# Kernel tuning notes

Hardware: AMD Instinct MI355X
Metric: run time of the kernel (lower is better)

Reference implementation:

```python
import jax, jax.numpy as jnp
import numpy as np

DIM = 4096
NUM_HEAD = 32
NUM_KV_HEAD = 8
ROPE_THETA = 10000.0
B, T = 2, 2048


def apply_rope(x, start_pos=0, theta=ROPE_THETA):
    # x: [B, T, H, d_head]; rotate half-split pairs by position-dependent angles
    d = x.shape[-1]
    half = d // 2
    inv_freq = 1.0 / (theta ** (jnp.arange(0, half, dtype=jnp.float32) / half))
    pos = jnp.arange(x.shape[1], dtype=jnp.float32) + start_pos  # [T]
    ang = pos[:, None] * inv_freq[None, :]                       # [T, half]
    cos = jnp.cos(ang)[None, :, None, :]
    sin = jnp.sin(ang)[None, :, None, :]
    x1, x2 = x[..., :half], x[..., half:]
    return jnp.concatenate([x1 * cos - x2 * sin, x1 * sin + x2 * cos], axis=-1)


def setup_inputs() -> dict:
    key = jax.random.key(0)
    ks = jax.random.split(key, 5)
    scale = 0.02
    X = jax.random.normal(ks[0], (B, T, DIM), dtype=jnp.float32)
    Wq = jax.random.normal(ks[1], (DIM, DIM), dtype=jnp.float32) * scale
    Wk = jax.random.normal(ks[2], (DIM, DIM // NUM_HEAD * NUM_KV_HEAD), dtype=jnp.float32) * scale
    Wv = jax.random.normal(ks[3], (DIM, DIM // NUM_HEAD * NUM_KV_HEAD), dtype=jnp.float32) * scale
    Wo = jax.random.normal(ks[4], (DIM, DIM), dtype=jnp.float32) * scale
    return {"X": X, "Wq": Wq, "Wk": Wk, "Wv": Wv, "Wo": Wo}


def reference(X, Wq, Wk, Wv, Wo):
    Bs, Ts, C = X.shape
    H, Hkv = NUM_HEAD, NUM_KV_HEAD
    dh = C // H
    G = H // Hkv  # GQA group size

    Q = apply_rope((X @ Wq).reshape(Bs, Ts, H, dh))      # [B,T,H,dh]
    K = apply_rope((X @ Wk).reshape(Bs, Ts, Hkv, dh))    # [B,T,Hkv,dh]
    V = (X @ Wv).reshape(Bs, Ts, Hkv, dh)                # [B,T,Hkv,dh]

    # [B,Hkv,G,T,dh]: grouped layout equivalent to repeat_interleave on head dim
    Qh = Q.transpose(0, 2, 1, 3).reshape(Bs, Hkv, G, Ts, dh)
    Kh = K.transpose(0, 2, 1, 3)  # [B,Hkv,T,dh]
    Vh = V.transpose(0, 2, 1, 3)

    scores = jnp.einsum('bkgtd,bksd->bkgts', Qh, Kh) / jnp.sqrt(jnp.float32(dh))
    causal = jnp.tril(jnp.ones((Ts, Ts), dtype=bool))
    scores = jnp.where(causal[None, None, None], scores, -jnp.inf)
    attn = jax.nn.softmax(scores, axis=-1)
    out = jnp.einsum('bkgts,bksd->bkgtd', attn, Vh)       # [B,Hkv,G,T,dh]
    out = out.reshape(Bs, H, Ts, dh).transpose(0, 2, 1, 3).reshape(Bs, Ts, C)
    return out @ Wo
```

## Files before the change

kernel.cpp:

```cpp
#include <hip/hip_runtime.h>
#include <hip/hip_bf16.h>
#include <cstdint>
#include <cstddef>

#define B_   2
#define T_   2048
#define DIM_ 4096
#define H_   32
#define HKV_ 8
#define DH_  128
#define MROWS (B_*T_)

typedef __bf16 bf16_t;
typedef bf16_t bf16x8 __attribute__((ext_vector_type(8)));
typedef bf16_t bf16x4 __attribute__((ext_vector_type(4)));
typedef float  f32x4  __attribute__((ext_vector_type(4)));

typedef __attribute__((address_space(1))) void gvoid_t;
typedef __attribute__((address_space(3))) void lvoid_t;

__device__ __forceinline__ void gld_lds16(const void* g, void* l) {
  __builtin_amdgcn_global_load_lds((gvoid_t*)g, (lvoid_t*)l, 16, 0, 0);
}

__device__ __forceinline__ f32x4 mfma16(bf16x8 a, bf16x8 b, f32x4 c) {
  return __builtin_amdgcn_mfma_f32_16x16x32_bf16(a, b, c, 0, 0, 0);
}

__global__ void cast_f32_bf16(const float* __restrict__ in,
                              bf16_t* __restrict__ out, int n4) {
  int i = blockIdx.x * blockDim.x + threadIdx.x;
  if (i < n4) {
    float4 v = ((const float4*)in)[i];
    bf16x4 o;
    o[0] = (bf16_t)v.x; o[1] = (bf16_t)v.y; o[2] = (bf16_t)v.z; o[3] = (bf16_t)v.w;
    ((bf16x4*)out)[i] = o;
  }
}

__global__ void transpose_cast(const float* __restrict__ in,
                               bf16_t* __restrict__ out, int K, int N) {
  __shared__ float tile[32][33];
  int n0 = blockIdx.x * 32, k0 = blockIdx.y * 32;
  int tx = threadIdx.x, ty = threadIdx.y;
#pragma unroll
  for (int j = 0; j < 4; ++j)
    tile[ty + j*8][tx] = in[(size_t)(k0 + ty + j*8) * N + n0 + tx];
  __syncthreads();
#pragma unroll
  for (int j = 0; j < 4; ++j)
    out[(size_t)(n0 + ty + j*8) * K + k0 + tx] = (bf16_t)tile[tx][ty + j*8];
}

template <int OUT_F32>
__global__ __launch_bounds__(256, 2)
void gemm_bt(const bf16_t* __restrict__ A, const bf16_t* __restrict__ BT,
             void* __restrict__ C, int M, int N, int K) {
  __shared__ __align__(16) bf16_t Als[128 * 32];
  __shared__ __align__(16) bf16_t Bls[128 * 32];
  const int tid  = threadIdx.x;
  const int wave = tid >> 6, lane = tid & 63;
  const int quad = lane >> 4, l16 = lane & 15;
  const int wm = wave >> 1, wn = wave & 1;
  const int m0 = blockIdx.y * 128, n0 = blockIdx.x * 128;

  f32x4 acc[4][4] = {};

  const int srow = lane >> 2;
  const int scol = (lane & 3) * 8;

  for (int k0 = 0; k0 < K; k0 += 32) {
#pragma unroll
    for (int c = 0; c < 2; ++c) {
      int ch = wave * 2 + c;
      gld_lds16(A + (size_t)(m0 + ch*16 + srow) * K + k0 + scol,
                &Als[ch*512 + srow*32 + scol]);
    }
#pragma unroll
    for (int c = 0; c < 2; ++c) {
      int ch = wave * 2 + c;
      gld_lds16(BT + (size_t)(n0 + ch*16 + srow) * K + k0 + scol,
                &Bls[ch*512 + srow*32 + scol]);
    }
    __syncthreads();

    bf16x8 af[4], bfr[4];
#pragma unroll
    for (int mi = 0; mi < 4; ++mi)
      af[mi] = *(const bf16x8*)&Als[(wm*64 + mi*16 + l16)*32 + quad*8];
#pragma unroll
    for (int ni = 0; ni < 4; ++ni)
      bfr[ni] = *(const bf16x8*)&Bls[(wn*64 + ni*16 + l16)*32 + quad*8];
#pragma unroll
    for (int mi = 0; mi < 4; ++mi)
#pragma unroll
      for (int ni = 0; ni < 4; ++ni)
        acc[mi][ni] = mfma16(af[mi], bfr[ni], acc[mi][ni]);
    __syncthreads();
  }

#pragma unroll
  for (int mi = 0; mi < 4; ++mi)
#pragma unroll
    for (int ni = 0; ni < 4; ++ni)
#pragma unroll
      for (int r = 0; r < 4; ++r) {
        int row = m0 + wm*64 + mi*16 + quad*4 + r;
        int col = n0 + wn*64 + ni*16 + l16;
        if (OUT_F32)
          ((float*)C)[(size_t)row * N + col] = acc[mi][ni][r];
        else
          ((bf16_t*)C)[(size_t)row * N + col] = (bf16_t)acc[mi][ni][r];
      }
}

__global__ void rope_kernel(bf16_t* __restrict__ X, int Hn, int total) {
  int i = blockIdx.x * blockDim.x + threadIdx.x;
  if (i >= total) return;
  int d   = i & 63;
  int rem = i >> 6;
  int h   = rem % Hn; rem /= Hn;
  int t   = rem % T_;
  int b   = rem / T_;
  size_t base = ((size_t)(b * T_ + t) * Hn + h) * DH_;
  float x1 = (float)X[base + d];
  float x2 = (float)X[base + 64 + d];
  float inv_freq = expf(-(float)d * 0.14391156758f);
  float ang = (float)t * inv_freq;
  float s, c;
  sincosf(ang, &s, &c);
  X[base + d]      = (bf16_t)(x1 * c - x2 * s);
  X[base + 64 + d] = (bf16_t)(x1 * s + x2 * c);
}

__global__ void v_transpose(const bf16_t* __restrict__ Vb,
                            bf16_t* __restrict__ VT) {
  __shared__ bf16_t tile[32][33];
  int t0 = blockIdx.x * 32;
  int d0 = blockIdx.y * 32;
  int bk = blockIdx.z;
  int b = bk >> 3, kv = bk & 7;
  int tx = threadIdx.x, ty = threadIdx.y;
#pragma unroll
  for (int j = 0; j < 4; ++j)
    tile[ty + j*8][tx] =
        Vb[(size_t)(b * T_ + t0 + ty + j*8) * (HKV_*DH_) + kv*DH_ + d0 + tx];
  __syncthreads();
#pragma unroll
  for (int j = 0; j < 4; ++j)
    VT[((size_t)bk * DH_ + d0 + ty + j*8) * T_ + t0 + tx] = tile[tx][ty + j*8];
}

__global__ __launch_bounds__(256, 2)
void flash_attn(const bf16_t* __restrict__ Qb, const bf16_t* __restrict__ Kb,
                const bf16_t* __restrict__ VT, bf16_t* __restrict__ Ob) {
  __shared__ __align__(16) bf16_t Kls[64 * 128];
  __shared__ __align__(16) bf16_t Vls[128 * 64];
  __shared__ __align__(16) bf16_t Pls[128 * 72];

  const int tid = threadIdx.x, wave = tid >> 6, lane = tid & 63;
  const int quad = lane >> 4, l16 = lane & 15;
  const int qt = blockIdx.x, h = blockIdx.y, b = blockIdx.z;
  const int kv = h >> 2;

  bf16x8 q[2][4];
#pragma unroll
  for (int mi = 0; mi < 2; ++mi) {
    const bf16_t* base =
        Qb + (size_t)(b*T_ + qt*128 + wave*32 + mi*16 + l16) * DIM_ + h*DH_;
#pragma unroll
    for (int kk = 0; kk < 4; ++kk)
      q[mi][kk] = *(const bf16x8*)(base + kk*32 + quad*8);
  }

  float m_st[2][4], l_st[2][4];
  f32x4 o_acc[2][8] = {};
#pragma unroll
  for (int mi = 0; mi < 2; ++mi)
#pragma unroll
    for (int r = 0; r < 4; ++r) { m_st[mi][r] = -3e38f; l_st[mi][r] = 0.f; }

  const int nkv = 2 * (qt + 1);
  for (int kvt = 0; kvt < nkv; ++kvt) {
    __syncthreads();

    {
      int r_in = lane >> 4, cphys = lane & 15;
#pragma unroll
      for (int c = 0; c < 4; ++c) {
        int ch = wave * 4 + c;
        int krow = ch * 4 + r_in;
        int clog = cphys ^ (krow & 7);
        gld_lds16(Kb + (size_t)(b*T_ + kvt*64 + krow) * (HKV_*DH_) + kv*DH_ + clog*8,
                  &Kls[ch*512 + lane*8]);
      }
      int r8 = lane >> 3, c8 = lane & 7;
#pragma unroll
      for (int c = 0; c < 4; ++c) {
        int ch = wave * 4 + c;
        int drow = ch * 8 + r8;
        int clog = c8 ^ (drow & 7);
        gld_lds16(VT + ((size_t)(b*HKV_ + kv) * DH_ + drow) * T_ + kvt*64 + clog*8,
                  &Vls[ch*512 + lane*8]);
      }
    }
    __syncthreads();

    f32x4 s[2][4] = {};
#pragma unroll
    for (int kk = 0; kk < 4; ++kk) {
      bf16x8 kf[4];
#pragma unroll
      for (int ni = 0; ni < 4; ++ni) {
        int krow = ni*16 + l16;
        int cphys = (kk*4 + quad) ^ (krow & 7);
        kf[ni] = *(const bf16x8*)&Kls[krow*128 + cphys*8];
      }
#pragma unroll
      for (int mi = 0; mi < 2; ++mi)
#pragma unroll
        for (int ni = 0; ni < 4; ++ni)
          s[mi][ni] = mfma16(q[mi][kk], kf[ni], s[mi][ni]);
    }

    const float sc = 0.08838834764831845f;
    const bool need_mask = (kvt >= 2*qt);
#pragma unroll
    for (int mi = 0; mi < 2; ++mi) {
      float al[4];
#pragma unroll
      for (int r = 0; r < 4; ++r) {
        int rpos = qt*128 + wave*32 + mi*16 + quad*4 + r;
        float mx = -3e38f;
#pragma unroll
        for (int ni = 0; ni < 4; ++ni) {
          float v = s[mi][ni][r] * sc;
          if (need_mask) {
            int cpos = kvt*64 + ni*16 + l16;
            if (cpos > rpos) v = -3e38f;
          }
          s[mi][ni][r] = v;
          mx = fmaxf(mx, v);
        }
#pragma unroll
        for (int off = 1; off < 16; off <<= 1)
          mx = fmaxf(mx, __shfl_xor(mx, off, 64));
        float mnew = fmaxf(m_st[mi][r], mx);
        float alpha = __expf(m_st[mi][r] - mnew);
        m_st[mi][r] = mnew;
        float rs = 0.f;
#pragma unroll
        for (int ni = 0; ni < 4; ++ni) {
          float p = __expf(s[mi][ni][r] - mnew);
          s[mi][ni][r] = p;
          rs += p;
        }
#pragma unroll
        for (int off = 1; off < 16; off <<= 1)
          rs += __shfl_xor(rs, off, 64);
        l_st[mi][r] = l_st[mi][r] * alpha + rs;
        al[r] = alpha;
      }
#pragma unroll
      for (int ni = 0; ni < 8; ++ni)
#pragma unroll
        for (int r = 0; r < 4; ++r) o_acc[mi][ni][r] *= al[r];
#pragma unroll
      for (int ni = 0; ni < 4; ++ni)
#pragma unroll
        for (int r = 0; r < 4; ++r) {
          int prow = wave*32 + mi*16 + quad*4 + r;
          Pls[prow*72 + ni*16 + l16] = (bf16_t)s[mi][ni][r];
        }
    }
    __syncthreads();

#pragma unroll
    for (int kk = 0; kk < 2; ++kk) {
      bf16x8 pf[2], vf[8];
#pragma unroll
      for (int mi = 0; mi < 2; ++mi) {
        int prow = wave*32 + mi*16 + l16;
        pf[mi] = *(const bf16x8*)&Pls[prow*72 + kk*32 + quad*8];
      }
#pragma unroll
      for (int ni = 0; ni < 8; ++ni) {
        int drow = ni*16 + l16;
        int cphys = (kk*4 + quad) ^ (drow & 7);
        vf[ni] = *(const bf16x8*)&Vls[drow*64 + cphys*8];
      }
#pragma unroll
      for (int mi = 0; mi < 2; ++mi)
#pragma unroll
        for (int ni = 0; ni < 8; ++ni)
          o_acc[mi][ni] = mfma16(pf[mi], vf[ni], o_acc[mi][ni]);
    }
  }

#pragma unroll
  for (int mi = 0; mi < 2; ++mi) {
    float inv[4];
#pragma unroll
    for (int r = 0; r < 4; ++r) inv[r] = 1.f / l_st[mi][r];
#pragma unroll
    for (int ni = 0; ni < 8; ++ni)
#pragma unroll
      for (int r = 0; r < 4; ++r) {
        size_t row = (size_t)(b*T_ + qt*128 + wave*32 + mi*16 + quad*4 + r);
        int col = h*DH_ + ni*16 + l16;
        Ob[row * DIM_ + col] = (bf16_t)(o_acc[mi][ni][r] * inv[r]);
      }
  }
}

extern "C" void kernel_launch(void* const* d_in, const int* in_sizes, int n_in,
                              void* d_out, int out_size, void* d_ws, size_t ws_size,
                              hipStream_t stream) {
  const float* X  = (const float*)d_in[0];
  const float* Wq = (const float*)d_in[1];
  const float* Wk = (const float*)d_in[2];
  const float* Wv = (const float*)d_in[3];
  const float* Wo = (const float*)d_in[4];
  float* out = (float*)d_out;

  char* ws = (char*)d_ws;
  const size_t SZ_X  = (size_t)MROWS * DIM_ * 2;
  const size_t SZ_WQ = (size_t)DIM_ * DIM_ * 2;
  const size_t SZ_WK = (size_t)DIM_ * 1024 * 2;
  bf16_t* Xb  = (bf16_t*)(ws);
  bf16_t* WqT = (bf16_t*)(ws + SZ_X);
  bf16_t* WkT = (bf16_t*)(ws + SZ_X + SZ_WQ);
  bf16_t* WvT = (bf16_t*)(ws + SZ_X + SZ_WQ + SZ_WK);
  bf16_t* WoT = (bf16_t*)(ws + SZ_X + SZ_WQ + 2*SZ_WK);
  bf16_t* Qb  = (bf16_t*)(ws + SZ_X + 2*SZ_WQ + 2*SZ_WK);
  bf16_t* Kb  = (bf16_t*)(ws + 2*SZ_X + 2*SZ_WQ + 2*SZ_WK);
  bf16_t* Vb  = (bf16_t*)(ws + 2*SZ_X + 2*SZ_WQ + 3*SZ_WK);
  bf16_t* VT  = (bf16_t*)(ws + 2*SZ_X + 2*SZ_WQ + 4*SZ_WK);
  bf16_t* Ob  = Xb;

  {
    int n4 = MROWS * DIM_ / 4;
    cast_f32_bf16<<<(n4 + 255)/256, 256, 0, stream>>>(X, Xb, n4);
  }
  transpose_cast<<<dim3(DIM_/32, DIM_/32), dim3(32,8), 0, stream>>>(Wq, WqT, DIM_, DIM_);
  transpose_cast<<<dim3(1024/32, DIM_/32), dim3(32,8), 0, stream>>>(Wk, WkT, DIM_, 1024);
  transpose_cast<<<dim3(1024/32, DIM_/32), dim3(32,8), 0, stream>>>(Wv, WvT, DIM_, 1024);
  transpose_cast<<<dim3(DIM_/32, DIM_/32), dim3(32,8), 0, stream>>>(Wo, WoT, DIM_, DIM_);

  gemm_bt<0><<<dim3(DIM_/128, MROWS/128), 256, 0, stream>>>(Xb, WqT, Qb, MROWS, DIM_, DIM_);
  gemm_bt<0><<<dim3(1024/128, MROWS/128), 256, 0, stream>>>(Xb, WkT, Kb, MROWS, 1024, DIM_);
  gemm_bt<0><<<dim3(1024/128, MROWS/128), 256, 0, stream>>>(Xb, WvT, Vb, MROWS, 1024, DIM_);

  {
    int totq = B_ * T_ * H_ * 64;
    rope_kernel<<<(totq + 255)/256, 256, 0, stream>>>(Qb, H_, totq);
    int totk = B_ * T_ * HKV_ * 64;
    rope_kernel<<<(totk + 255)/256, 256, 0, stream>>>(Kb, HKV_, totk);
  }

  v_transpose<<<dim3(T_/32, DH_/32, B_*HKV_), dim3(32,8), 0, stream>>>(Vb, VT);

  flash_attn<<<dim3(T_/128, H_, B_), 256, 0, stream>>>(Qb, Kb, VT, Ob);

  gemm_bt<1><<<dim3(DIM_/128, MROWS/128), 256, 0, stream>>>(Ob, WoT, out, MROWS, DIM_, DIM_);
}
```

Before: 993.7 us.

## Fuse QKV projections into one GEMM and restructure flash attention

```diff
diff --git a/kernel.cpp b/kernel.cpp
--- a/kernel.cpp
+++ b/kernel.cpp
@@ -10,14 +10,24 @@
 #define HKV_ 8
 #define DH_  128
 #define MROWS (B_*T_)
+#define QS_   6144
+#define KOFF_ 4096
+#define VOFF_ 5120
 
 typedef __bf16 bf16_t;
 typedef bf16_t bf16x8 __attribute__((ext_vector_type(8)));
 typedef bf16_t bf16x4 __attribute__((ext_vector_type(4)));
+typedef bf16_t bf16x2 __attribute__((ext_vector_type(2)));
 typedef float  f32x4  __attribute__((ext_vector_type(4)));
 
 typedef __attribute__((address_space(1))) void gvoid_t;
 typedef __attribute__((address_space(3))) void lvoid_t;
+
+#if __has_builtin(__builtin_amdgcn_exp2f)
+#define EXP2F(x) __builtin_amdgcn_exp2f(x)
+#else
+#define EXP2F(x) exp2f(x)
+#endif
 
 __device__ __forceinline__ void gld_lds16(const void* g, void* l) {
   __builtin_amdgcn_global_load_lds((gvoid_t*)g, (lvoid_t*)l, 16, 0, 0);
@@ -65,7 +75,6 @@
   const int m0 = blockIdx.y * 128, n0 = blockIdx.x * 128;
 
   f32x4 acc[4][4] = {};
-
   const int srow = lane >> 2;
   const int scol = (lane & 3) * 8;
 
@@ -114,7 +123,8 @@
       }
 }
 
-__global__ void rope_kernel(bf16_t* __restrict__ X, int Hn, int total) {
+__global__ void rope_kernel(bf16_t* __restrict__ X, int Hn, int rowStr,
+                            int headOff, int total) {
   int i = blockIdx.x * blockDim.x + threadIdx.x;
   if (i >= total) return;
   int d   = i & 63;
@@ -122,7 +132,7 @@
   int h   = rem % Hn; rem /= Hn;
   int t   = rem % T_;
   int b   = rem / T_;
-  size_t base = ((size_t)(b * T_ + t) * Hn + h) * DH_;
+  size_t base = (size_t)(b * T_ + t) * rowStr + headOff + h * DH_;
   float x1 = (float)X[base + d];
   float x2 = (float)X[base + 64 + d];
   float inv_freq = expf(-(float)d * 0.14391156758f);
@@ -133,7 +143,7 @@
   X[base + 64 + d] = (bf16_t)(x1 * s + x2 * c);
 }
 
-__global__ void v_transpose(const bf16_t* __restrict__ Vb,
+__global__ void v_transpose(const bf16_t* __restrict__ Vin,
                             bf16_t* __restrict__ VT) {
   __shared__ bf16_t tile[32][33];
   int t0 = blockIdx.x * 32;
@@ -144,62 +154,57 @@
 #pragma unroll
   for (int j = 0; j < 4; ++j)
     tile[ty + j*8][tx] =
-        Vb[(size_t)(b * T_ + t0 + ty + j*8) * (HKV_*DH_) + kv*DH_ + d0 + tx];
+        Vin[(size_t)(b * T_ + t0 + ty + j*8) * QS_ + kv*DH_ + d0 + tx];
   __syncthreads();
 #pragma unroll
   for (int j = 0; j < 4; ++j)
     VT[((size_t)bk * DH_ + d0 + ty + j*8) * T_ + t0 + tx] = tile[tx][ty + j*8];
 }
 
-__global__ __launch_bounds__(256, 2)
-void flash_attn(const bf16_t* __restrict__ Qb, const bf16_t* __restrict__ Kb,
-                const bf16_t* __restrict__ VT, bf16_t* __restrict__ Ob) {
+__global__ __launch_bounds__(256, 3)
+void flash_attn(const bf16_t* __restrict__ QKV, const bf16_t* __restrict__ VT,
+                bf16_t* __restrict__ Ob) {
   __shared__ __align__(16) bf16_t Kls[64 * 128];
   __shared__ __align__(16) bf16_t Vls[128 * 64];
-  __shared__ __align__(16) bf16_t Pls[128 * 72];
 
   const int tid = threadIdx.x, wave = tid >> 6, lane = tid & 63;
   const int quad = lane >> 4, l16 = lane & 15;
-  const int qt = blockIdx.x, h = blockIdx.y, b = blockIdx.z;
+  const int idx = blockIdx.x;
+  const int qt = 15 - (idx & 15);
+  const int h  = (idx >> 4) & 31;
+  const int b  = idx >> 9;
   const int kv = h >> 2;
 
+  const float CSC = 0.12751744642f;
+
   bf16x8 q[2][4];
 #pragma unroll
-  for (int mi = 0; mi < 2; ++mi) {
+  for (int qb = 0; qb < 2; ++qb) {
     const bf16_t* base =
-        Qb + (size_t)(b*T_ + qt*128 + wave*32 + mi*16 + l16) * DIM_ + h*DH_;
+        QKV + (size_t)(b*T_ + qt*128 + wave*32 + qb*16 + l16) * QS_ + h*DH_;
 #pragma unroll
     for (int kk = 0; kk < 4; ++kk)
-      q[mi][kk] = *(const bf16x8*)(base + kk*32 + quad*8);
-  }
-
-  float m_st[2][4], l_st[2][4];
-  f32x4 o_acc[2][8] = {};
-#pragma unroll
-  for (int mi = 0; mi < 2; ++mi)
-#pragma unroll
-    for (int r = 0; r < 4; ++r) { m_st[mi][r] = -3e38f; l_st[mi][r] = 0.f; }
+      q[qb][kk] = *(const bf16x8*)(base + kk*32 + quad*8);
+  }
+
+  float m_st[2] = {-3e38f, -3e38f}, l_st[2] = {0.f, 0.f};
+  f32x4 o_acc[8][2] = {};
 
   const int nkv = 2 * (qt + 1);
   for (int kvt = 0; kvt < nkv; ++kvt) {
     __syncthreads();
-
     {
-      int r_in = lane >> 4, cphys = lane & 15;
+      int r_in = lane >> 4, cph = lane & 15;
 #pragma unroll
       for (int c = 0; c < 4; ++c) {
-        int ch = wave * 4 + c;
-        int krow = ch * 4 + r_in;
-        int clog = cphys ^ (krow & 7);
-        gld_lds16(Kb + (size_t)(b*T_ + kvt*64 + krow) * (HKV_*DH_) + kv*DH_ + clog*8,
+        int ch = wave*4 + c, krow = ch*4 + r_in, clog = cph ^ (krow & 7);
+        gld_lds16(QKV + (size_t)(b*T_ + kvt*64 + krow) * QS_ + KOFF_ + kv*DH_ + clog*8,
                   &Kls[ch*512 + lane*8]);
       }
       int r8 = lane >> 3, c8 = lane & 7;
 #pragma unroll
       for (int c = 0; c < 4; ++c) {
-        int ch = wave * 4 + c;
-        int drow = ch * 8 + r8;
-        int clog = c8 ^ (drow & 7);
+        int ch = wave*4 + c, drow = ch*8 + r8, clog = c8 ^ (drow & 7);
         gld_lds16(VT + ((size_t)(b*HKV_ + kv) * DH_ + drow) * T_ + kvt*64 + clog*8,
                   &Vls[ch*512 + lane*8]);
       }
@@ -211,104 +216,108 @@
     for (int kk = 0; kk < 4; ++kk) {
       bf16x8 kf[4];
 #pragma unroll
-      for (int ni = 0; ni < 4; ++ni) {
-        int krow = ni*16 + l16;
-        int cphys = (kk*4 + quad) ^ (krow & 7);
-        kf[ni] = *(const bf16x8*)&Kls[krow*128 + cphys*8];
-      }
-#pragma unroll
-      for (int mi = 0; mi < 2; ++mi)
-#pragma unroll
-        for (int ni = 0; ni < 4; ++ni)
-          s[mi][ni] = mfma16(q[mi][kk], kf[ni], s[mi][ni]);
-    }
-
-    const float sc = 0.08838834764831845f;
+      for (int nb = 0; nb < 4; ++nb) {
+        int krow = nb*16 + l16;
+        int pc = (kk*4 + quad) ^ (krow & 7);
+        kf[nb] = *(const bf16x8*)&Kls[krow*128 + pc*8];
+      }
+#pragma unroll
+      for (int qb = 0; qb < 2; ++qb)
+#pragma unroll
+        for (int nb = 0; nb < 4; ++nb)
+          s[qb][nb] = mfma16(kf[nb], q[qb][kk], s[qb][nb]);
+    }
+
     const bool need_mask = (kvt >= 2*qt);
-#pragma unroll
-    for (int mi = 0; mi < 2; ++mi) {
-      float al[4];
-#pragma unroll
-      for (int r = 0; r < 4; ++r) {
-        int rpos = qt*128 + wave*32 + mi*16 + quad*4 + r;
-        float mx = -3e38f;
-#pragma unroll
-        for (int ni = 0; ni < 4; ++ni) {
-          float v = s[mi][ni][r] * sc;
-          if (need_mask) {
-            int cpos = kvt*64 + ni*16 + l16;
-            if (cpos > rpos) v = -3e38f;
-          }
-          s[mi][ni][r] = v;
-          mx = fmaxf(mx, v);
-        }
-#pragma unroll
-        for (int off = 1; off < 16; off <<= 1)
-          mx = fmaxf(mx, __shfl_xor(mx, off, 64));
-        float mnew = fmaxf(m_st[mi][r], mx);
-        float alpha = __expf(m_st[mi][r] - mnew);
-        m_st[mi][r] = mnew;
-        float rs = 0.f;
-#pragma unroll
-        for (int ni = 0; ni < 4; ++ni) {
-          float p = __expf(s[mi][ni][r] - mnew);
-          s[mi][ni][r] = p;
+    union PU { uint32_t u[4]; bf16x8 v; };
+    PU pb[2][2];
+
+#pragma unroll
+    for (int qb = 0; qb < 2; ++qb) {
+      if (need_mask) {
+        int qpos = qt*128 + wave*32 + qb*16 + l16;
+#pragma unroll
+        for (int nb = 0; nb < 4; ++nb)
+#pragma unroll
+          for (int r = 0; r < 4; ++r)
+            if (kvt*64 + nb*16 + quad*4 + r > qpos) s[qb][nb][r] = -3e38f;
+      }
+      float mx = -3e38f;
+#pragma unroll
+      for (int nb = 0; nb < 4; ++nb)
+#pragma unroll
+        for (int r = 0; r < 4; ++r) mx = fmaxf(mx, s[qb][nb][r]);
+      mx = fmaxf(mx, __shfl_xor(mx, 16, 64));
+      mx = fmaxf(mx, __shfl_xor(mx, 32, 64));
+      float mnew = fmaxf(m_st[qb], mx);
+      float alpha = EXP2F((m_st[qb] - mnew) * CSC);
+      m_st[qb] = mnew;
+      float mc = mnew * CSC;
+      float rs = 0.f;
+#pragma unroll
+      for (int nb = 0; nb < 4; ++nb)
+#pragma unroll
+        for (int r = 0; r < 4; ++r) {
+          float p = EXP2F(fmaf(s[qb][nb][r], CSC, -mc));
+          s[qb][nb][r] = p;
           rs += p;
         }
-#pragma unroll
-        for (int off = 1; off < 16; off <<= 1)
-          rs += __shfl_xor(rs, off, 64);
-        l_st[mi][r] = l_st[mi][r] * alpha + rs;
-        al[r] = alpha;
-      }
-#pragma unroll
-      for (int ni = 0; ni < 8; ++ni)
-#pragma unroll
-        for (int r = 0; r < 4; ++r) o_acc[mi][ni][r] *= al[r];
-#pragma unroll
-      for (int ni = 0; ni < 4; ++ni)
-#pragma unroll
-        for (int r = 0; r < 4; ++r) {
-          int prow = wave*32 + mi*16 + quad*4 + r;
-          Pls[prow*72 + ni*16 + l16] = (bf16_t)s[mi][ni][r];
+      rs += __shfl_xor(rs, 16, 64);
+      rs += __shfl_xor(rs, 32, 64);
+      l_st[qb] = l_st[qb] * alpha + rs;
+#pragma unroll
+      for (int dhb = 0; dhb < 8; ++dhb) o_acc[dhb][qb] *= alpha;
+
+      uint32_t pk2[4][2];
+#pragma unroll
+      for (int nb = 0; nb < 4; ++nb)
+#pragma unroll
+        for (int rp = 0; rp < 2; ++rp) {
+          union BU { bf16x2 v; uint32_t u; } bu;
+          bu.v[0] = (bf16_t)s[qb][nb][2*rp];
+          bu.v[1] = (bf16_t)s[qb][nb][2*rp+1];
+          pk2[nb][rp] = bu.u;
         }
-    }
-    __syncthreads();
-
-#pragma unroll
-    for (int kk = 0; kk < 2; ++kk) {
-      bf16x8 pf[2], vf[8];
-#pragma unroll
-      for (int mi = 0; mi < 2; ++mi) {
-        int prow = wave*32 + mi*16 + l16;
-        pf[mi] = *(const bf16x8*)&Pls[prow*72 + kk*32 + quad*8];
-      }
-#pragma unroll
-      for (int ni = 0; ni < 8; ++ni) {
-        int drow = ni*16 + l16;
-        int cphys = (kk*4 + quad) ^ (drow & 7);
-        vf[ni] = *(const bf16x8*)&Vls[drow*64 + cphys*8];
-      }
-#pragma unroll
-      for (int mi = 0; mi < 2; ++mi)
-#pragma unroll
-        for (int ni = 0; ni < 8; ++ni)
-          o_acc[mi][ni] = mfma16(pf[mi], vf[ni], o_acc[mi][ni]);
-    }
-  }
-
-#pragma unroll
-  for (int mi = 0; mi < 2; ++mi) {
-    float inv[4];
-#pragma unroll
-    for (int r = 0; r < 4; ++r) inv[r] = 1.f / l_st[mi][r];
-#pragma unroll
-    for (int ni = 0; ni < 8; ++ni)
-#pragma unroll
-      for (int r = 0; r < 4; ++r) {
-        size_t row = (size_t)(b*T_ + qt*128 + wave*32 + mi*16 + quad*4 + r);
-        int col = h*DH_ + ni*16 + l16;
-        Ob[row * DIM_ + col] = (bf16_t)(o_acc[mi][ni][r] * inv[r]);
+#pragma unroll
+      for (int kb = 0; kb < 2; ++kb)
+#pragma unroll
+        for (int k = 0; k < 4; ++k) {
+          uint32_t x = pk2[2*kb + ((quad & 1) ^ (k >> 1))][k & 1];
+          int src = (2*(quad & 1) + ((k >> 1) ^ (quad >> 1))) * 16 + l16;
+          uint32_t got = (uint32_t)__shfl((int)x, src, 64);
+          pb[qb][kb].u[k ^ ((quad >> 1) << 1)] = got;
+        }
+    }
+
+#pragma unroll
+    for (int dhb = 0; dhb < 8; ++dhb) {
+      bf16x8 vf[2];
+      int drow = dhb*16 + l16;
+#pragma unroll
+      for (int kb = 0; kb < 2; ++kb) {
+        int pc = (kb*4 + quad) ^ (drow & 7);
+        vf[kb] = *(const bf16x8*)&Vls[drow*64 + pc*8];
+      }
+#pragma unroll
+      for (int qb = 0; qb < 2; ++qb)
+#pragma unroll
+        for (int kb = 0; kb < 2; ++kb)
+          o_acc[dhb][qb] = mfma16(vf[kb], pb[qb][kb].v, o_acc[dhb][qb]);
+    }
+  }
+
+#pragma unroll
+  for (int qb = 0; qb < 2; ++qb) {
+    float inv = 1.f / l_st[qb];
+    size_t qrow = (size_t)(b*T_ + qt*128 + wave*32 + qb*16 + l16);
+#pragma unroll
+    for (int dhb = 0; dhb < 8; ++dhb)
+#pragma unroll
+      for (int rp = 0; rp < 2; ++rp) {
+        union BU { bf16x2 v; uint32_t u; } bu;
+        bu.v[0] = (bf16_t)(o_acc[dhb][qb][2*rp]   * inv);
+        bu.v[1] = (bf16_t)(o_acc[dhb][qb][2*rp+1] * inv);
+        *(uint32_t*)(Ob + qrow*DIM_ + h*DH_ + dhb*16 + quad*4 + 2*rp) = bu.u;
       }
   }
 }
@@ -324,43 +333,38 @@
   float* out = (float*)d_out;
 
   char* ws = (char*)d_ws;
-  const size_t SZ_X  = (size_t)MROWS * DIM_ * 2;
-  const size_t SZ_WQ = (size_t)DIM_ * DIM_ * 2;
-  const size_t SZ_WK = (size_t)DIM_ * 1024 * 2;
-  bf16_t* Xb  = (bf16_t*)(ws);
-  bf16_t* WqT = (bf16_t*)(ws + SZ_X);
-  bf16_t* WkT = (bf16_t*)(ws + SZ_X + SZ_WQ);
-  bf16_t* WvT = (bf16_t*)(ws + SZ_X + SZ_WQ + SZ_WK);
-  bf16_t* WoT = (bf16_t*)(ws + SZ_X + SZ_WQ + 2*SZ_WK);
-  bf16_t* Qb  = (bf16_t*)(ws + SZ_X + 2*SZ_WQ + 2*SZ_WK);
-  bf16_t* Kb  = (bf16_t*)(ws + 2*SZ_X + 2*SZ_WQ + 2*SZ_WK);
-  bf16_t* Vb  = (bf16_t*)(ws + 2*SZ_X + 2*SZ_WQ + 3*SZ_WK);
-  bf16_t* VT  = (bf16_t*)(ws + 2*SZ_X + 2*SZ_WQ + 4*SZ_WK);
-  bf16_t* Ob  = Xb;
+  const size_t SZ_X    = (size_t)MROWS * DIM_ * 2;
+  const size_t SZ_WQKV = (size_t)QS_ * DIM_ * 2;
+  const size_t SZ_WO   = (size_t)DIM_ * DIM_ * 2;
+  const size_t SZ_QKV  = (size_t)MROWS * QS_ * 2;
+  bf16_t* Xb    = (bf16_t*)(ws);
+  bf16_t* WT    = (bf16_t*)(ws + SZ_X);
+  bf16_t* WoT   = (bf16_t*)(ws + SZ_X + SZ_WQKV);
+  bf16_t* QKVb  = (bf16_t*)(ws + SZ_X + SZ_WQKV + SZ_WO);
+  bf16_t* VT    = (bf16_t*)(ws + SZ_X + SZ_WQKV + SZ_WO + SZ_QKV);
+  bf16_t* Ob    = Xb;
 
   {
     int n4 = MROWS * DIM_ / 4;
     cast_f32_bf16<<<(n4 + 255)/256, 256, 0, stream>>>(X, Xb, n4);
   }
-  transpose_cast<<<dim3(DIM_/32, DIM_/32), dim3(32,8), 0, stream>>>(Wq, WqT, DIM_, DIM_);
-  transpose_cast<<<dim3(1024/32, DIM_/32), dim3(32,8), 0, stream>>>(Wk, WkT, DIM_, 1024);
-  transpose_cast<<<dim3(1024/32, DIM_/32), dim3(32,8), 0, stream>>>(Wv, WvT, DIM_, 1024);
+  transpose_cast<<<dim3(DIM_/32, DIM_/32), dim3(32,8), 0, stream>>>(Wq, WT, DIM_, DIM_);
+  transpose_cast<<<dim3(1024/32, DIM_/32), dim3(32,8), 0, stream>>>(Wk, WT + (size_t)KOFF_*DIM_, DIM_, 1024);
+  transpose_cast<<<dim3(1024/32, DIM_/32), dim3(32,8), 0, stream>>>(Wv, WT + (size_t)VOFF_*DIM_, DIM_, 1024);
   transpose_cast<<<dim3(DIM_/32, DIM_/32), dim3(32,8), 0, stream>>>(Wo, WoT, DIM_, DIM_);
 
-  gemm_bt<0><<<dim3(DIM_/128, MROWS/128), 256, 0, stream>>>(Xb, WqT, Qb, MROWS, DIM_, DIM_);
-  gemm_bt<0><<<dim3(1024/128, MROWS/128), 256, 0, stream>>>(Xb, WkT, Kb, MROWS, 1024, DIM_);
-  gemm_bt<0><<<dim3(1024/128, MROWS/128), 256, 0, stream>>>(Xb, WvT, Vb, MROWS, 1024, DIM_);
+  gemm_bt<0><<<dim3(QS_/128, MROWS/128), 256, 0, stream>>>(Xb, WT, QKVb, MROWS, QS_, DIM_);
 
   {
     int totq = B_ * T_ * H_ * 64;
-    rope_kernel<<<(totq + 255)/256, 256, 0, stream>>>(Qb, H_, totq);
+    rope_kernel<<<(totq + 255)/256, 256, 0, stream>>>(QKVb, H_, QS_, 0, totq);
     int totk = B_ * T_ * HKV_ * 64;
-    rope_kernel<<<(totk + 255)/256, 256, 0, stream>>>(Kb, HKV_, totk);
-  }
-
-  v_transpose<<<dim3(T_/32, DH_/32, B_*HKV_), dim3(32,8), 0, stream>>>(Vb, VT);
-
-  flash_attn<<<dim3(T_/128, H_, B_), 256, 0, stream>>>(Qb, Kb, VT, Ob);
+    rope_kernel<<<(totk + 255)/256, 256, 0, stream>>>(QKVb, HKV_, QS_, KOFF_, totk);
+  }
+
+  v_transpose<<<dim3(T_/32, DH_/32, B_*HKV_), dim3(32,8), 0, stream>>>(QKVb + VOFF_, VT);
+
+  flash_attn<<<dim3(T_/128 * H_ * B_), 256, 0, stream>>>(QKVb, VT, Ob);
 
   gemm_bt<1><<<dim3(DIM_/128, MROWS/128), 256, 0, stream>>>(Ob, WoT, out, MROWS, DIM_, DIM_);
 }
```

Result: slower. 1.164 ms (+17.1%).
